# Optimization experiments

Hardware: AMD Instinct MI355X
Metric: run time of the kernel (lower is better)

The kernel has to match this reference:

```python
import jax, jax.numpy as jnp
import numpy as np

N, C_TOTAL, C, H, W = 8, 448, 100, 56, 56


def setup_inputs() -> dict:
    key = jax.random.key(0)
    k1, k2, k3, k4 = jax.random.split(key, 4)
    fmaps = jax.random.normal(k1, (N, C_TOTAL, H, W), dtype=jnp.float32)
    select_index = jax.random.randint(k2, (C,), 0, C_TOTAL)
    mean = jax.random.normal(k3, (C, H, W), dtype=jnp.float32)
    # Per-pixel inverse covariance must be PSD so the quadratic form is >= 0
    A = jax.random.normal(k4, (C, C, H, W), dtype=jnp.float32)
    cov = jnp.einsum('cehw,dehw->cdhw', A, A) / jnp.float32(C)  # (C,C,H,W), PSD per pixel
    return {
        'fmaps': fmaps,
        'select_index': select_index,
        'mean': mean,
        'cov': cov,
        'min_score': jnp.float32(0.0),
        'max_score': jnp.float32(50.0),
    }


def reference(fmaps, select_index, mean, cov, min_score, max_score):
    # x_ = fmaps[:, select_index, ...] - mean  -> (N, C, H, W)
    x = fmaps[:, select_index, :, :] - mean[None]
    # left = sum_c x[n,c,h,w] * cov[c,d,h,w]  (per-pixel matvec), avoids (N,C,C,H,W) intermediate
    left = jnp.einsum('nchw,cdhw->ndhw', x, cov)
    # per-pixel Mahalanobis distance
    s_map = jnp.sqrt(jnp.sum(x * left, axis=1))  # (N, H, W)
    # bilinear upsample x4 (torch Upsample align_corners=False == half-pixel linear resize)
    score_map = jax.image.resize(s_map, (s_map.shape[0], 4 * H, 4 * W), method='linear')
    scores = (score_map - min_score) / (max_score - min_score)
    return jnp.squeeze(scores)
```

## Files before the change

kernel.cpp:

```cpp
#include <hip/hip_runtime.h>
#include <math.h>

#define NN 8
#define C_TOTAL 448
#define CC 100
#define HH 56
#define WW 56
#define HW (HH*WW)
#define NPIX4 (HW/4)
#define OH 224
#define OW 224
#define NT4 13
#define NK 50

typedef __attribute__((ext_vector_type(4))) _Float16 half4;
typedef __attribute__((ext_vector_type(8))) _Float16 half8;
typedef __attribute__((ext_vector_type(4))) float    f32x4;

__device__ __forceinline__ f32x4 cvtlo(const half8 h) {
    return __builtin_convertvector(__builtin_shufflevector(h, h, 0, 1, 2, 3), f32x4);
}
__device__ __forceinline__ f32x4 cvthi(const half8 h) {
    return __builtin_convertvector(__builtin_shufflevector(h, h, 4, 5, 6, 7), f32x4);
}
__device__ __forceinline__ f32x4 fmav(const f32x4 a, const f32x4 b, const f32x4 c) {
    f32x4 r;
    r.x = fmaf(a.x, b.x, c.x);
    r.y = fmaf(a.y, b.y, c.y);
    r.z = fmaf(a.z, b.z, c.z);
    r.w = fmaf(a.w, b.w, c.w);
    return r;
}

__global__ __launch_bounds__(256) void prep_x_kernel(
    const float* __restrict__ fmaps, const int* __restrict__ sel,
    const float* __restrict__ mean, half4* __restrict__ xbuf,
    float* __restrict__ smap)
{
    const int idx = blockIdx.x * 256 + threadIdx.x;
    if (idx < NN * NPIX4) {
        ((float4*)smap)[idx] = make_float4(0.f, 0.f, 0.f, 0.f);
    }
    if (idx >= CC * NPIX4) return;
    const int quad = idx % NPIX4;
    const int c    = idx / NPIX4;

    const float4* f4 = (const float4*)fmaps;
    const float4  m  = ((const float4*)mean)[(size_t)c * NPIX4 + quad];
    const int     sc = sel[c];

    half4 hv[NN];
#pragma unroll
    for (int n = 0; n < NN; ++n) {
        const float4 f = f4[((size_t)n * C_TOTAL + sc) * NPIX4 + quad];
        half4 h;
        h.x = (_Float16)(f.x - m.x);
        h.y = (_Float16)(f.y - m.y);
        h.z = (_Float16)(f.z - m.z);
        h.w = (_Float16)(f.w - m.w);
        hv[n] = h;
    }
    half4* dst = xbuf + ((size_t)c * NPIX4 + quad) * NN;
#pragma unroll
    for (int n = 0; n < NN; ++n) dst[n] = hv[n];
}

__global__ __launch_bounds__(256, 5) void qform_kernel(
    const half4* __restrict__ xbuf, const float* __restrict__ cov,
    float* __restrict__ smap)
{
    __shared__ f32x4 lred[4 * 4 * 64];

    const int tile = blockIdx.x % NT4;
    const int rest = blockIdx.x / NT4;
    const int h    = rest & 1;
    const int k    = rest >> 1;
    const int a    = 2 * k;
    const int b    = a + 1;

    const int w    = threadIdx.x >> 6;
    const int dph  = w & 1;
    const int nh   = w >> 1;
    const int lane = threadIdx.x & 63;
    const int qraw = tile * 64 + lane;
    const bool valid = qraw < NPIX4;
    const int quad = valid ? qraw : (NPIX4 - 1);

    const int L   = CC - a;
    const int mid = a + ((L + 1) >> 1);
    const int dlo = h ? mid : a;
    const int dhi = h ? CC  : mid;

    const f32x4* c4 = (const f32x4*)cov;

    f32x4 acca[4], accb[4];
#pragma unroll
    for (int i = 0; i < 4; ++i) {
        acca[i] = (f32x4){0.f, 0.f, 0.f, 0.f};
        accb[i] = (f32x4){0.f, 0.f, 0.f, 0.f};
    }

    for (int d = dlo + dph; d < dhi; d += 2) {
        const half8* xp = (const half8*)(xbuf + ((size_t)d * NPIX4 + quad) * NN + nh * 4);
        const half8 hA = xp[0];
        const half8 hB = xp[1];
        f32x4 xv[4];
        xv[0] = cvtlo(hA); xv[1] = cvthi(hA);
        xv[2] = cvtlo(hB); xv[3] = cvthi(hB);

        f32x4 cva = __builtin_nontemporal_load(&c4[((size_t)a * CC + d) * NPIX4 + quad]);
        if (d == a) cva *= 0.5f;
#pragma unroll
        for (int i = 0; i < 4; ++i) acca[i] = fmav(xv[i], cva, acca[i]);

        if (d > a) {
            f32x4 cvb = __builtin_nontemporal_load(&c4[((size_t)b * CC + d) * NPIX4 + quad]);
            if (d == b) cvb *= 0.5f;
#pragma unroll
            for (int i = 0; i < 4; ++i) accb[i] = fmav(xv[i], cvb, accb[i]);
        }
    }

    {
        const half8* xap = (const half8*)(xbuf + ((size_t)a * NPIX4 + quad) * NN + nh * 4);
        const half8* xbp = (const half8*)(xbuf + ((size_t)b * NPIX4 + quad) * NN + nh * 4);
        const half8 xa0 = xap[0], xa1 = xap[1];
        const half8 xb0 = xbp[0], xb1 = xbp[1];
        f32x4 xa[4], xb[4];
        xa[0] = cvtlo(xa0); xa[1] = cvthi(xa0); xa[2] = cvtlo(xa1); xa[3] = cvthi(xa1);
        xb[0] = cvtlo(xb0); xb[1] = cvthi(xb0); xb[2] = cvtlo(xb1); xb[3] = cvthi(xb1);
#pragma unroll
        for (int i = 0; i < 4; ++i) {
            f32x4 t = xa[i] * acca[i];
            t = fmav(xb[i], accb[i], t);
            t = t + t;
            lred[(w * 4 + i) * 64 + lane] = t;
        }
    }
    __syncthreads();

#pragma unroll
    for (int j = 0; j < 2; ++j) {
        const int im  = 2 * w + j;
        const int nhh = im >> 2;
        const int sl  = im & 3;
        const f32x4 s0 = lred[((nhh * 2 + 0) * 4 + sl) * 64 + lane];
        const f32x4 s1 = lred[((nhh * 2 + 1) * 4 + sl) * 64 + lane];
        const f32x4 s  = s0 + s1;
        if (valid) {
            float* dst = smap + (size_t)im * HW + (size_t)qraw * 4;
            atomicAdd(dst + 0, s.x);
            atomicAdd(dst + 1, s.y);
            atomicAdd(dst + 2, s.z);
            atomicAdd(dst + 3, s.w);
        }
    }
}

__global__ __launch_bounds__(256) void upsample_kernel(
    const float* __restrict__ smap,
    const float* __restrict__ minp, const float* __restrict__ maxp,
    float* __restrict__ out)
{
    const int idx = blockIdx.x * 256 + threadIdx.x;
    const int total = NN * OH * OW;
    if (idx >= total) return;

    const int ox = idx % OW;
    const int oy = (idx / OW) % OH;
    const int n  = idx / (OW * OH);

    const float fy = oy * 0.25f - 0.375f;
    const float fx = ox * 0.25f - 0.375f;

    int y0 = (int)floorf(fy);
    int x0 = (int)floorf(fx);
    const float wy = fy - (float)y0;
    const float wx = fx - (float)x0;
    int y1 = min(y0 + 1, HH - 1); y0 = max(y0, 0);
    int x1 = min(x0 + 1, WW - 1); x0 = max(x0, 0);

    const float* s = smap + (size_t)n * HW;
    const float v00 = sqrtf(fmaxf(s[y0 * WW + x0], 0.f));
    const float v01 = sqrtf(fmaxf(s[y0 * WW + x1], 0.f));
    const float v10 = sqrtf(fmaxf(s[y1 * WW + x0], 0.f));
    const float v11 = sqrtf(fmaxf(s[y1 * WW + x1], 0.f));

    const float v = (1.0f - wy) * ((1.0f - wx) * v00 + wx * v01)
                  +          wy * ((1.0f - wx) * v10 + wx * v11);

    const float mn = *minp;
    const float mx = *maxp;
    out[idx] = (v - mn) / (mx - mn);
}

extern "C" void kernel_launch(void* const* d_in, const int* in_sizes, int n_in,
                              void* d_out, int out_size, void* d_ws, size_t ws_size,
                              hipStream_t stream)
{
    const float* fmaps = (const float*)d_in[0];
    const int*   sel   = (const int*)  d_in[1];
    const float* mean  = (const float*)d_in[2];
    const float* cov   = (const float*)d_in[3];
    const float* minp  = (const float*)d_in[4];
    const float* maxp  = (const float*)d_in[5];
    float* out = (float*)d_out;

    half4* xbuf = (half4*)d_ws;
    float* smap = (float*)((char*)d_ws + (size_t)CC*NPIX4*NN*8);

    {
        const int total = CC * NPIX4;
        prep_x_kernel<<<(total + 255) / 256, 256, 0, stream>>>(fmaps, sel, mean, xbuf, smap);
    }
    qform_kernel<<<NK * 2 * NT4, 256, 0, stream>>>(xbuf, cov, smap);
    {
        const int total = NN * OH * OW;
        upsample_kernel<<<(total + 255) / 256, 256, 0, stream>>>(smap, minp, maxp, out);
    }
}
```

Measured before the change: 233.5 us.

## Process four cov rows per block to quadruple x reuse in quadratic form

```diff
diff --git a/kernel.cpp b/kernel.cpp
--- a/kernel.cpp
+++ b/kernel.cpp
@@ -11,7 +11,7 @@
 #define OH 224
 #define OW 224
 #define NT4 13
-#define NK 50
+#define NG 25
 
 typedef __attribute__((ext_vector_type(4))) _Float16 half4;
 typedef __attribute__((ext_vector_type(8))) _Float16 half8;
@@ -65,88 +65,100 @@
     for (int n = 0; n < NN; ++n) dst[n] = hv[n];
 }
 
-__global__ __launch_bounds__(256, 5) void qform_kernel(
+__global__ __launch_bounds__(512, 3) void qform_kernel(
     const half4* __restrict__ xbuf, const float* __restrict__ cov,
     float* __restrict__ smap)
 {
-    __shared__ f32x4 lred[4 * 4 * 64];
+    __shared__ f32x4 lred[8 * 4 * 64];
 
     const int tile = blockIdx.x % NT4;
-    const int rest = blockIdx.x / NT4;
-    const int h    = rest & 1;
-    const int k    = rest >> 1;
-    const int a    = 2 * k;
-    const int b    = a + 1;
+    const int k    = blockIdx.x / NT4;
+    const int a    = 4 * k;
 
     const int w    = threadIdx.x >> 6;
-    const int dph  = w & 1;
-    const int nh   = w >> 1;
+    const int dph  = w & 3;
+    const int imgh = w >> 2;
     const int lane = threadIdx.x & 63;
     const int qraw = tile * 64 + lane;
     const bool valid = qraw < NPIX4;
     const int quad = valid ? qraw : (NPIX4 - 1);
 
-    const int L   = CC - a;
-    const int mid = a + ((L + 1) >> 1);
-    const int dlo = h ? mid : a;
-    const int dhi = h ? CC  : mid;
-
     const f32x4* c4 = (const f32x4*)cov;
 
-    f32x4 acca[4], accb[4];
-#pragma unroll
-    for (int i = 0; i < 4; ++i) {
-        acca[i] = (f32x4){0.f, 0.f, 0.f, 0.f};
-        accb[i] = (f32x4){0.f, 0.f, 0.f, 0.f};
-    }
-
-    for (int d = dlo + dph; d < dhi; d += 2) {
-        const half8* xp = (const half8*)(xbuf + ((size_t)d * NPIX4 + quad) * NN + nh * 4);
+    f32x4 acc[4][4];
+#pragma unroll
+    for (int i = 0; i < 4; ++i)
+#pragma unroll
+        for (int j = 0; j < 4; ++j) acc[i][j] = (f32x4){0.f, 0.f, 0.f, 0.f};
+
+    {
+        const int d0 = a + dph;
+        const half8* xp = (const half8*)(xbuf + ((size_t)d0 * NPIX4 + quad) * NN + imgh * 4);
         const half8 hA = xp[0];
         const half8 hB = xp[1];
         f32x4 xv[4];
         xv[0] = cvtlo(hA); xv[1] = cvthi(hA);
         xv[2] = cvtlo(hB); xv[3] = cvthi(hB);
-
-        f32x4 cva = __builtin_nontemporal_load(&c4[((size_t)a * CC + d) * NPIX4 + quad]);
-        if (d == a) cva *= 0.5f;
-#pragma unroll
-        for (int i = 0; i < 4; ++i) acca[i] = fmav(xv[i], cva, acca[i]);
-
-        if (d > a) {
-            f32x4 cvb = __builtin_nontemporal_load(&c4[((size_t)b * CC + d) * NPIX4 + quad]);
-            if (d == b) cvb *= 0.5f;
-#pragma unroll
-            for (int i = 0; i < 4; ++i) accb[i] = fmav(xv[i], cvb, accb[i]);
-        }
-    }
-
-    {
-        const half8* xap = (const half8*)(xbuf + ((size_t)a * NPIX4 + quad) * NN + nh * 4);
-        const half8* xbp = (const half8*)(xbuf + ((size_t)b * NPIX4 + quad) * NN + nh * 4);
-        const half8 xa0 = xap[0], xa1 = xap[1];
-        const half8 xb0 = xbp[0], xb1 = xbp[1];
-        f32x4 xa[4], xb[4];
-        xa[0] = cvtlo(xa0); xa[1] = cvthi(xa0); xa[2] = cvtlo(xa1); xa[3] = cvthi(xa1);
-        xb[0] = cvtlo(xb0); xb[1] = cvthi(xb0); xb[2] = cvtlo(xb1); xb[3] = cvthi(xb1);
 #pragma unroll
         for (int i = 0; i < 4; ++i) {
-            f32x4 t = xa[i] * acca[i];
-            t = fmav(xb[i], accb[i], t);
-            t = t + t;
-            lred[(w * 4 + i) * 64 + lane] = t;
+            if (i <= dph) {
+                f32x4 cv = __builtin_nontemporal_load(
+                    &c4[((size_t)(a + i) * CC + d0) * NPIX4 + quad]);
+                if (i == dph) cv *= 0.5f;
+#pragma unroll
+                for (int j = 0; j < 4; ++j) acc[i][j] = fmav(xv[j], cv, acc[i][j]);
+            }
+        }
+    }
+
+    for (int d = a + 4 + dph; d < CC; d += 4) {
+        const half8* xp = (const half8*)(xbuf + ((size_t)d * NPIX4 + quad) * NN + imgh * 4);
+        const half8 hA = xp[0];
+        const half8 hB = xp[1];
+        f32x4 xv[4];
+        xv[0] = cvtlo(hA); xv[1] = cvthi(hA);
+        xv[2] = cvtlo(hB); xv[3] = cvthi(hB);
+
+        const size_t base = ((size_t)a * CC + d) * NPIX4 + quad;
+#pragma unroll
+        for (int i = 0; i < 4; ++i) {
+            const f32x4 cv = __builtin_nontemporal_load(&c4[base + (size_t)i * CC * NPIX4]);
+#pragma unroll
+            for (int j = 0; j < 4; ++j) acc[i][j] = fmav(xv[j], cv, acc[i][j]);
+        }
+    }
+
+    {
+        f32x4 part[4];
+#pragma unroll
+        for (int j = 0; j < 4; ++j) part[j] = (f32x4){0.f, 0.f, 0.f, 0.f};
+#pragma unroll
+        for (int i = 0; i < 4; ++i) {
+            const half8* xp = (const half8*)(xbuf + ((size_t)(a + i) * NPIX4 + quad) * NN + imgh * 4);
+            const half8 hA = xp[0];
+            const half8 hB = xp[1];
+            part[0] = fmav(cvtlo(hA), acc[i][0], part[0]);
+            part[1] = fmav(cvthi(hA), acc[i][1], part[1]);
+            part[2] = fmav(cvtlo(hB), acc[i][2], part[2]);
+            part[3] = fmav(cvthi(hB), acc[i][3], part[3]);
+        }
+#pragma unroll
+        for (int j = 0; j < 4; ++j) {
+            part[j] = part[j] + part[j];
+            lred[(w * 4 + j) * 64 + lane] = part[j];
         }
     }
     __syncthreads();
 
-#pragma unroll
-    for (int j = 0; j < 2; ++j) {
-        const int im  = 2 * w + j;
-        const int nhh = im >> 2;
-        const int sl  = im & 3;
-        const f32x4 s0 = lred[((nhh * 2 + 0) * 4 + sl) * 64 + lane];
-        const f32x4 s1 = lred[((nhh * 2 + 1) * 4 + sl) * 64 + lane];
-        const f32x4 s  = s0 + s1;
+    {
+        const int im = w;
+        const int ih = im >> 2;
+        const int sl = im & 3;
+        f32x4 s = (f32x4){0.f, 0.f, 0.f, 0.f};
+#pragma unroll
+        for (int dp = 0; dp < 4; ++dp) {
+            s = s + lred[((ih * 4 + dp) * 4 + sl) * 64 + lane];
+        }
         if (valid) {
             float* dst = smap + (size_t)im * HW + (size_t)qraw * 4;
             atomicAdd(dst + 0, s.x);
@@ -213,7 +225,7 @@
         const int total = CC * NPIX4;
         prep_x_kernel<<<(total + 255) / 256, 256, 0, stream>>>(fmaps, sel, mean, xbuf, smap);
     }
-    qform_kernel<<<NK * 2 * NT4, 256, 0, stream>>>(xbuf, cov, smap);
+    qform_kernel<<<NG * NT4, 512, 0, stream>>>(xbuf, cov, smap);
     {
         const int total = NN * OH * OW;
         upsample_kernel<<<(total + 255) / 256, 256, 0, stream>>>(smap, minp, maxp, out);
```

Result: faster. 221.8 us (-5.0%).
